# Optimization experiments

Measured on AMD Instinct MI355X. Metric: run time of the kernel, lower is better.

## Reference

```python
import jax, jax.numpy as jnp
import numpy as np

B = 8192          # batch_size (pairs of embeddings)
D = 1024          # embedding dim
C = 1024          # number of classes (torch.unique(labels) -> 0..C-1, all present)
EPS = 1e-12       # F.normalize eps


def _normalize(x):
    # F.normalize(x, dim=1): x / max(||x||_2, eps)
    n = jnp.linalg.norm(x, axis=1, keepdims=True)
    return x / jnp.maximum(n, EPS)


def setup_inputs() -> dict:
    key = jax.random.key(0)
    k1, k2, k3 = jax.random.split(key, 3)
    emb_i = jax.random.normal(k1, (B, D), dtype=jnp.float32)
    emb_j = jax.random.normal(k2, (B, D), dtype=jnp.float32)
    # shuffled arange % C guarantees every class id in [0, C) appears,
    # matching torch.unique(labels) == arange(C)
    labels = jax.random.permutation(k3, jnp.arange(B, dtype=jnp.int32) % C).astype(jnp.int64)
    return {"emb_i": emb_i, "emb_j": emb_j, "labels": labels}


def reference(emb_i, emb_j, labels):
    z_i = _normalize(emb_i)  # [B, D]
    z_j = _normalize(emb_j)  # [B, D]

    # vectorized replacement of the per-label python loop:
    # class_prototypes[c] = mean of z_i rows with label c  (segment mean)
    seg_sum = jax.ops.segment_sum(z_i, labels, num_segments=C)                    # [C, D]
    seg_cnt = jax.ops.segment_sum(jnp.ones((B,), z_i.dtype), labels, num_segments=C)  # [C]
    prototypes = seg_sum / seg_cnt[:, None]                                       # [C, D]

    # similarity = 2 - cdist(z_j, prototypes, p=2)
    d2 = (jnp.sum(z_j * z_j, axis=1)[:, None]
          + jnp.sum(prototypes * prototypes, axis=1)[None, :]
          - 2.0 * z_j @ prototypes.T)                                             # [B, C]
    sim = 2.0 - jnp.sqrt(jnp.maximum(d2, 0.0))

    # match_matrix: labels_proto (arange(C)) == labels[:, None]
    match = (jnp.arange(C)[None, :] == labels[:, None]).astype(sim.dtype)         # [B, C]

    # BCEWithLogitsLoss (mean reduction), numerically stable via log_sigmoid
    loss = jnp.mean(-(match * jax.nn.log_sigmoid(sim)
                      + (1.0 - match) * jax.nn.log_sigmoid(-sim)))
    return loss
```

## Files before the change

kernel.cpp:

```cpp
#include <hip/hip_runtime.h>

#define B_N 8192
#define D_N 1024
#define C_N 1024

typedef __attribute__((ext_vector_type(8))) __bf16 bf16x8;
typedef __attribute__((ext_vector_type(4))) float floatx4;

__device__ inline unsigned short f2bf(float f) {
  union { float f; unsigned int u; } cv; cv.f = f;
  unsigned int b = cv.u;
  unsigned int r = (b + 0x7FFFu + ((b >> 16) & 1u)) >> 16;
  return (unsigned short)r;
}

__global__ __launch_bounds__(256) void normj_idx_kernel(
    const float* __restrict__ emb_j, const int* __restrict__ labels,
    unsigned short* __restrict__ z_j, int* __restrict__ cnt,
    int* __restrict__ idx) {
  __shared__ float sred[4];
  const int row = blockIdx.x;

  if (threadIdx.x == 0) {
    const int lab = labels[row];
    const int pos = atomicAdd(&cnt[lab], 1) & 7;
    idx[lab * 8 + pos] = row;
  }

  const float4 v = ((const float4*)(emb_j + (size_t)row * D_N))[threadIdx.x];
  float ss = v.x * v.x + v.y * v.y + v.z * v.z + v.w * v.w;
  for (int o = 32; o; o >>= 1) ss += __shfl_xor(ss, o, 64);
  if ((threadIdx.x & 63) == 0) sred[threadIdx.x >> 6] = ss;
  __syncthreads();
  const float tot = sred[0] + sred[1] + sred[2] + sred[3];
  const float inv = 1.0f / fmaxf(sqrtf(tot), 1e-12f);

  ushort4 u;
  u.x = f2bf(v.x * inv); u.y = f2bf(v.y * inv);
  u.z = f2bf(v.z * inv); u.w = f2bf(v.w * inv);
  ((ushort4*)(z_j + (size_t)row * D_N))[threadIdx.x] = u;
}

__global__ __launch_bounds__(256) void proto_kernel(
    const float* __restrict__ emb_i, const int* __restrict__ idx,
    unsigned short* __restrict__ proto, float* __restrict__ p2) {
  __shared__ float sred[4][8];
  __shared__ float sinv[8];
  __shared__ int sidx[8];
  const int t = threadIdx.x;
  const int c = blockIdx.x;
  if (t < 8) sidx[t] = idx[c * 8 + t];
  __syncthreads();

  float4 v[8];
  float ss[8];
#pragma unroll
  for (int k = 0; k < 8; ++k) {
    v[k] = ((const float4*)(emb_i + (size_t)sidx[k] * D_N))[t];
    ss[k] = v[k].x * v[k].x + v[k].y * v[k].y + v[k].z * v[k].z + v[k].w * v[k].w;
  }
#pragma unroll
  for (int k = 0; k < 8; ++k)
    for (int o = 32; o; o >>= 1) ss[k] += __shfl_xor(ss[k], o, 64);
  if ((t & 63) == 0) {
#pragma unroll
    for (int k = 0; k < 8; ++k) sred[t >> 6][k] = ss[k];
  }
  __syncthreads();
  if (t < 8) {
    const float tot = sred[0][t] + sred[1][t] + sred[2][t] + sred[3][t];
    sinv[t] = 1.0f / fmaxf(sqrtf(tot), 1e-12f);
  }
  __syncthreads();

  float4 acc = make_float4(0.f, 0.f, 0.f, 0.f);
#pragma unroll
  for (int k = 0; k < 8; ++k) {
    const float iv = sinv[k];
    acc.x += v[k].x * iv; acc.y += v[k].y * iv;
    acc.z += v[k].z * iv; acc.w += v[k].w * iv;
  }
  acc.x *= 0.125f; acc.y *= 0.125f; acc.z *= 0.125f; acc.w *= 0.125f;

  float s2 = acc.x * acc.x + acc.y * acc.y + acc.z * acc.z + acc.w * acc.w;
  for (int o = 32; o; o >>= 1) s2 += __shfl_xor(s2, o, 64);
  __syncthreads();
  if ((t & 63) == 0) sred[t >> 6][0] = s2;
  __syncthreads();
  if (t == 0) p2[c] = sred[0][0] + sred[1][0] + sred[2][0] + sred[3][0];

  ushort4 u;
  u.x = f2bf(acc.x); u.y = f2bf(acc.y);
  u.z = f2bf(acc.z); u.w = f2bf(acc.w);
  ((ushort4*)(proto + (size_t)c * D_N))[threadIdx.x] = u;
}

#define BM 128
#define BN 128
#define BK 64

__global__ __launch_bounds__(256) void gemm_loss_kernel(
    const unsigned short* __restrict__ Zj,
    const unsigned short* __restrict__ P,
    const float* __restrict__ p2,
    const int* __restrict__ labels,
    float* __restrict__ out) {
  __shared__ __align__(16) unsigned short As[BM * BK];
  __shared__ __align__(16) unsigned short Bs[BN * BK];
  __shared__ float sred[4];

  const int t = threadIdx.x;
  const int lane = t & 63;
  const int wid = t >> 6;
  const int wm = (wid >> 1) * 64;
  const int wn = (wid & 1) * 64;
  const int bm = blockIdx.x;
  const int bn = blockIdx.y;

  floatx4 acc[4][4];
#pragma unroll
  for (int i = 0; i < 4; ++i)
#pragma unroll
    for (int j = 0; j < 4; ++j)
      acc[i][j] = (floatx4){0.f, 0.f, 0.f, 0.f};

  const int srow = t >> 3;
  const int scol = (((t & 7) ^ (srow & 7)) << 3);
  const unsigned short* Ag = Zj + (size_t)(bm * BM + srow) * D_N + scol;
  const unsigned short* Bg = P + (size_t)(bn * BN + srow) * D_N + scol;
  unsigned short* Al = As + t * 8;
  unsigned short* Bl = Bs + t * 8;

  for (int k0 = 0; k0 < D_N; k0 += BK) {
#pragma unroll
    for (int it = 0; it < 4; ++it) {
      __builtin_amdgcn_global_load_lds(
          (const __attribute__((address_space(1))) void*)(Ag + (size_t)it * 32 * D_N + k0),
          (__attribute__((address_space(3))) void*)(Al + it * 2048), 16, 0, 0);
      __builtin_amdgcn_global_load_lds(
          (const __attribute__((address_space(1))) void*)(Bg + (size_t)it * 32 * D_N + k0),
          (__attribute__((address_space(3))) void*)(Bl + it * 2048), 16, 0, 0);
    }
    __syncthreads();
#pragma unroll
    for (int kk = 0; kk < BK; kk += 32) {
      const int swz = ((((kk >> 3) + (lane >> 4)) ^ (lane & 7)) << 3);
      bf16x8 af[4], bfr[4];
#pragma unroll
      for (int mi = 0; mi < 4; ++mi)
        af[mi] = *(const bf16x8*)(As + (wm + mi * 16 + (lane & 15)) * BK + swz);
#pragma unroll
      for (int ni = 0; ni < 4; ++ni)
        bfr[ni] = *(const bf16x8*)(Bs + (wn + ni * 16 + (lane & 15)) * BK + swz);
#pragma unroll
      for (int mi = 0; mi < 4; ++mi)
#pragma unroll
        for (int ni = 0; ni < 4; ++ni)
          acc[mi][ni] = __builtin_amdgcn_mfma_f32_16x16x32_bf16(af[mi], bfr[ni], acc[mi][ni], 0, 0, 0);
    }
    __syncthreads();
  }

  const int colb = bn * BN + wn + (lane & 15);
  const int rowb = bm * BM + wm + ((lane >> 4) << 2);
  float p2c[4];
#pragma unroll
  for (int ni = 0; ni < 4; ++ni) p2c[ni] = p2[colb + ni * 16];

  float lsum = 0.f;
#pragma unroll
  for (int mi = 0; mi < 4; ++mi) {
#pragma unroll
    for (int r = 0; r < 4; ++r) {
      const int row = rowb + mi * 16 + r;
      const int lab = labels[row];
#pragma unroll
      for (int ni = 0; ni < 4; ++ni) {
        const float dot = acc[mi][ni][r];
        const float d2 = 1.0f + p2c[ni] - 2.0f * dot;
        const float s = 2.0f - sqrtf(fmaxf(d2, 0.0f));
        const float sp = fmaxf(s, 0.0f) + log1pf(expf(-fabsf(s)));
        lsum += sp - ((lab == colb + ni * 16) ? s : 0.0f);
      }
    }
  }
  for (int o = 32; o; o >>= 1) lsum += __shfl_xor(lsum, o, 64);
  if (lane == 0) sred[wid] = lsum;
  __syncthreads();
  if (t == 0)
    atomicAdd(out, (sred[0] + sred[1] + sred[2] + sred[3]) *
                       (1.0f / ((float)B_N * (float)C_N)));
}

extern "C" void kernel_launch(void* const* d_in, const int* in_sizes, int n_in,
                              void* d_out, int out_size, void* d_ws, size_t ws_size,
                              hipStream_t stream) {
  const float* emb_i = (const float*)d_in[0];
  const float* emb_j = (const float*)d_in[1];
  const int* labels = (const int*)d_in[2];
  float* out = (float*)d_out;

  char* ws = (char*)d_ws;
  unsigned short* z_j = (unsigned short*)ws;
  unsigned short* proto = (unsigned short*)(ws + (size_t)16777216);
  float* p2 = (float*)(ws + (size_t)18874368);
  int* cnt = (int*)(ws + (size_t)18878464);
  int* idx = (int*)(ws + (size_t)18882560);

  hipMemsetAsync(cnt, 0, C_N * sizeof(int), stream);
  hipMemsetAsync(out, 0, sizeof(float), stream);
  normj_idx_kernel<<<dim3(B_N), 256, 0, stream>>>(emb_j, labels, z_j, cnt, idx);
  proto_kernel<<<dim3(C_N), 256, 0, stream>>>(emb_i, idx, proto, p2);
  gemm_loss_kernel<<<dim3(B_N / BM, C_N / BN), 256, 0, stream>>>(z_j, proto, p2, labels, out);
}
```

Baseline: 151.8 us.

## Fuse normalize, prototype and GEMM-loss kernels into one persistent kernel with grid barriers

Merges the three kernels into a single 512-block persistent kernel that synchronises phases with software grid barriers, built on atomic counters in workspace. Each block now normalizes 16 z_j rows, builds 2 prototypes with half a row per wave, and then computes one 128x128 GEMM+loss tile. The aim is to remove two kernel launch gaps and their tail effects. In exchange it depends on all 512 blocks being co-resident (launch_bounds 256,3), or the barrier deadlocks. It also adds an extra memset and spin-wait cost.

```diff
diff --git a/kernel.cpp b/kernel.cpp
--- a/kernel.cpp
+++ b/kernel.cpp
@@ -3,6 +3,10 @@
 #define B_N 8192
 #define D_N 1024
 #define C_N 1024
+#define GRID 512
+#define BM 128
+#define BN 128
+#define BK 64
 
 typedef __attribute__((ext_vector_type(8))) __bf16 bf16x8;
 typedef __attribute__((ext_vector_type(4))) float floatx4;
@@ -13,121 +17,141 @@
   unsigned int r = (b + 0x7FFFu + ((b >> 16) & 1u)) >> 16;
   return (unsigned short)r;
 }
-
-__global__ __launch_bounds__(256) void normj_idx_kernel(
-    const float* __restrict__ emb_j, const int* __restrict__ labels,
-    unsigned short* __restrict__ z_j, int* __restrict__ cnt,
-    int* __restrict__ idx) {
+__device__ inline float d4(const float4 a) {
+  return a.x * a.x + a.y * a.y + a.z * a.z + a.w * a.w;
+}
+__device__ inline ushort4 pk4(const float4 v, const float s) {
+  ushort4 u;
+  u.x = f2bf(v.x * s); u.y = f2bf(v.y * s);
+  u.z = f2bf(v.z * s); u.w = f2bf(v.w * s);
+  return u;
+}
+
+__device__ inline void grid_barrier(int* counter) {
+  __syncthreads();
+  if (threadIdx.x == 0) {
+    __threadfence();
+    __hip_atomic_fetch_add(counter, 1, __ATOMIC_RELEASE, __HIP_MEMORY_SCOPE_AGENT);
+    while (__hip_atomic_load(counter, __ATOMIC_ACQUIRE, __HIP_MEMORY_SCOPE_AGENT) < GRID)
+      __builtin_amdgcn_s_sleep(1);
+    __threadfence();
+  }
+  __syncthreads();
+}
+
+__global__ __launch_bounds__(256, 3) void fused_kernel(
+    const float* __restrict__ emb_i, const float* __restrict__ emb_j,
+    const int* __restrict__ labels,
+    unsigned short* __restrict__ z_j, unsigned short* __restrict__ proto,
+    float* __restrict__ p2, int* __restrict__ cnt, int* __restrict__ idx,
+    int* __restrict__ bar, float* __restrict__ out) {
+  __shared__ __align__(16) unsigned short As[BM * BK];
+  __shared__ __align__(16) unsigned short Bs[BN * BK];
+  __shared__ float sx[4][8];
   __shared__ float sred[4];
-  const int row = blockIdx.x;
-
-  if (threadIdx.x == 0) {
+
+  const int t = threadIdx.x;
+  const int lane = t & 63;
+  const int wid = t >> 6;
+  const int blk = blockIdx.x;
+
+  if (t < 16) {
+    const int row = blk * 16 + t;
     const int lab = labels[row];
     const int pos = atomicAdd(&cnt[lab], 1) & 7;
     idx[lab * 8 + pos] = row;
   }
-
-  const float4 v = ((const float4*)(emb_j + (size_t)row * D_N))[threadIdx.x];
-  float ss = v.x * v.x + v.y * v.y + v.z * v.z + v.w * v.w;
-  for (int o = 32; o; o >>= 1) ss += __shfl_xor(ss, o, 64);
-  if ((threadIdx.x & 63) == 0) sred[threadIdx.x >> 6] = ss;
-  __syncthreads();
-  const float tot = sred[0] + sred[1] + sred[2] + sred[3];
-  const float inv = 1.0f / fmaxf(sqrtf(tot), 1e-12f);
-
-  ushort4 u;
-  u.x = f2bf(v.x * inv); u.y = f2bf(v.y * inv);
-  u.z = f2bf(v.z * inv); u.w = f2bf(v.w * inv);
-  ((ushort4*)(z_j + (size_t)row * D_N))[threadIdx.x] = u;
-}
-
-__global__ __launch_bounds__(256) void proto_kernel(
-    const float* __restrict__ emb_i, const int* __restrict__ idx,
-    unsigned short* __restrict__ proto, float* __restrict__ p2) {
-  __shared__ float sred[4][8];
-  __shared__ float sinv[8];
-  __shared__ int sidx[8];
-  const int t = threadIdx.x;
-  const int c = blockIdx.x;
-  if (t < 8) sidx[t] = idx[c * 8 + t];
-  __syncthreads();
-
-  float4 v[8];
-  float ss[8];
-#pragma unroll
-  for (int k = 0; k < 8; ++k) {
-    v[k] = ((const float4*)(emb_i + (size_t)sidx[k] * D_N))[t];
-    ss[k] = v[k].x * v[k].x + v[k].y * v[k].y + v[k].z * v[k].z + v[k].w * v[k].w;
-  }
-#pragma unroll
-  for (int k = 0; k < 8; ++k)
-    for (int o = 32; o; o >>= 1) ss[k] += __shfl_xor(ss[k], o, 64);
-  if ((t & 63) == 0) {
-#pragma unroll
-    for (int k = 0; k < 8; ++k) sred[t >> 6][k] = ss[k];
-  }
-  __syncthreads();
-  if (t < 8) {
-    const float tot = sred[0][t] + sred[1][t] + sred[2][t] + sred[3][t];
-    sinv[t] = 1.0f / fmaxf(sqrtf(tot), 1e-12f);
-  }
-  __syncthreads();
-
-  float4 acc = make_float4(0.f, 0.f, 0.f, 0.f);
-#pragma unroll
-  for (int k = 0; k < 8; ++k) {
-    const float iv = sinv[k];
-    acc.x += v[k].x * iv; acc.y += v[k].y * iv;
-    acc.z += v[k].z * iv; acc.w += v[k].w * iv;
-  }
-  acc.x *= 0.125f; acc.y *= 0.125f; acc.z *= 0.125f; acc.w *= 0.125f;
-
-  float s2 = acc.x * acc.x + acc.y * acc.y + acc.z * acc.z + acc.w * acc.w;
-  for (int o = 32; o; o >>= 1) s2 += __shfl_xor(s2, o, 64);
-  __syncthreads();
-  if ((t & 63) == 0) sred[t >> 6][0] = s2;
-  __syncthreads();
-  if (t == 0) p2[c] = sred[0][0] + sred[1][0] + sred[2][0] + sred[3][0];
-
-  ushort4 u;
-  u.x = f2bf(acc.x); u.y = f2bf(acc.y);
-  u.z = f2bf(acc.z); u.w = f2bf(acc.w);
-  ((ushort4*)(proto + (size_t)c * D_N))[threadIdx.x] = u;
-}
-
-#define BM 128
-#define BN 128
-#define BK 64
-
-__global__ __launch_bounds__(256) void gemm_loss_kernel(
-    const unsigned short* __restrict__ Zj,
-    const unsigned short* __restrict__ P,
-    const float* __restrict__ p2,
-    const int* __restrict__ labels,
-    float* __restrict__ out) {
-  __shared__ __align__(16) unsigned short As[BM * BK];
-  __shared__ __align__(16) unsigned short Bs[BN * BK];
-  __shared__ float sred[4];
-
-  const int t = threadIdx.x;
-  const int lane = t & 63;
-  const int wid = t >> 6;
+#pragma unroll
+  for (int r = 0; r < 4; ++r) {
+    const int row = blk * 16 + wid * 4 + r;
+    const float4* src = (const float4*)(emb_j + (size_t)row * D_N);
+    const float4 v0 = src[lane], v1 = src[lane + 64];
+    const float4 v2 = src[lane + 128], v3 = src[lane + 192];
+    float ss = d4(v0) + d4(v1) + d4(v2) + d4(v3);
+    for (int o = 32; o; o >>= 1) ss += __shfl_xor(ss, o, 64);
+    const float inv = 1.0f / fmaxf(sqrtf(ss), 1e-12f);
+    ushort4* dst = (ushort4*)(z_j + (size_t)row * D_N);
+    dst[lane] = pk4(v0, inv);
+    dst[lane + 64] = pk4(v1, inv);
+    dst[lane + 128] = pk4(v2, inv);
+    dst[lane + 192] = pk4(v3, inv);
+  }
+
+  grid_barrier(&bar[0]);
+
+  {
+    const int c = blk * 2 + (wid >> 1);
+    const int half = wid & 1;
+    const float* base = emb_i + half * 512;
+    float4 v0[8], v1[8];
+    float inv[8];
+    {
+      float ss[8];
+#pragma unroll
+      for (int k = 0; k < 8; ++k) {
+        const int row = idx[c * 8 + k];
+        const float4* src = (const float4*)(base + (size_t)row * D_N);
+        v0[k] = src[lane];
+        v1[k] = src[lane + 64];
+        ss[k] = d4(v0[k]) + d4(v1[k]);
+      }
+#pragma unroll
+      for (int k = 0; k < 8; ++k)
+        for (int o = 32; o; o >>= 1) ss[k] += __shfl_xor(ss[k], o, 64);
+      if (lane == 0) {
+#pragma unroll
+        for (int k = 0; k < 8; ++k) sx[wid][k] = ss[k];
+      }
+    }
+    __syncthreads();
+#pragma unroll
+    for (int k = 0; k < 8; ++k) {
+      const float tot = sx[wid][k] + sx[wid ^ 1][k];
+      inv[k] = 1.0f / fmaxf(sqrtf(tot), 1e-12f);
+    }
+    float4 a0 = make_float4(0.f, 0.f, 0.f, 0.f);
+    float4 a1 = make_float4(0.f, 0.f, 0.f, 0.f);
+#pragma unroll
+    for (int k = 0; k < 8; ++k) {
+      const float iv = inv[k];
+      a0.x += v0[k].x * iv; a0.y += v0[k].y * iv;
+      a0.z += v0[k].z * iv; a0.w += v0[k].w * iv;
+      a1.x += v1[k].x * iv; a1.y += v1[k].y * iv;
+      a1.z += v1[k].z * iv; a1.w += v1[k].w * iv;
+    }
+    a0.x *= 0.125f; a0.y *= 0.125f; a0.z *= 0.125f; a0.w *= 0.125f;
+    a1.x *= 0.125f; a1.y *= 0.125f; a1.z *= 0.125f; a1.w *= 0.125f;
+
+    float pp = d4(a0) + d4(a1);
+    for (int o = 32; o; o >>= 1) pp += __shfl_xor(pp, o, 64);
+    __syncthreads();
+    if (lane == 0) sx[wid][0] = pp;
+    __syncthreads();
+    if (lane == 0 && half == 0) p2[c] = sx[wid][0] + sx[wid ^ 1][0];
+
+    ushort4* dst = (ushort4*)(proto + (size_t)c * D_N + half * 512);
+    dst[lane] = pk4(a0, 1.0f);
+    dst[lane + 64] = pk4(a1, 1.0f);
+  }
+
+  grid_barrier(&bar[1]);
+
+  const int bm = blk & 63;
+  const int bn = blk >> 6;
+
+  floatx4 acc[4][4];
+#pragma unroll
+  for (int i = 0; i < 4; ++i)
+#pragma unroll
+    for (int j = 0; j < 4; ++j)
+      acc[i][j] = (floatx4){0.f, 0.f, 0.f, 0.f};
+
   const int wm = (wid >> 1) * 64;
   const int wn = (wid & 1) * 64;
-  const int bm = blockIdx.x;
-  const int bn = blockIdx.y;
-
-  floatx4 acc[4][4];
-#pragma unroll
-  for (int i = 0; i < 4; ++i)
-#pragma unroll
-    for (int j = 0; j < 4; ++j)
-      acc[i][j] = (floatx4){0.f, 0.f, 0.f, 0.f};
-
   const int srow = t >> 3;
   const int scol = (((t & 7) ^ (srow & 7)) << 3);
-  const unsigned short* Ag = Zj + (size_t)(bm * BM + srow) * D_N + scol;
-  const unsigned short* Bg = P + (size_t)(bn * BN + srow) * D_N + scol;
+  const unsigned short* Ag = z_j + (size_t)(bm * BM + srow) * D_N + scol;
+  const unsigned short* Bg = proto + (size_t)(bn * BN + srow) * D_N + scol;
   unsigned short* Al = As + t * 8;
   unsigned short* Bl = Bs + t * 8;
 
@@ -206,10 +230,11 @@
   float* p2 = (float*)(ws + (size_t)18874368);
   int* cnt = (int*)(ws + (size_t)18878464);
   int* idx = (int*)(ws + (size_t)18882560);
+  int* bar = (int*)(ws + (size_t)18915328);
 
   hipMemsetAsync(cnt, 0, C_N * sizeof(int), stream);
+  hipMemsetAsync(bar, 0, 2 * sizeof(int), stream);
   hipMemsetAsync(out, 0, sizeof(float), stream);
-  normj_idx_kernel<<<dim3(B_N), 256, 0, stream>>>(emb_j, labels, z_j, cnt, idx);
-  proto_kernel<<<dim3(C_N), 256, 0, stream>>>(emb_i, idx, proto, p2);
-  gemm_loss_kernel<<<dim3(B_N / BM, C_N / BN), 256, 0, stream>>>(z_j, proto, p2, labels, out);
-}
+  fused_kernel<<<dim3(GRID), 256, 0, stream>>>(emb_i, emb_j, labels, z_j,
+                                               proto, p2, cnt, idx, bar, out);
+}
```

New measurement: 269.5 us. 1.78x slower.
